# Performance work log

Hardware: AMD Instinct MI355X
Metric: run time of the kernel (lower is better)

Reference implementation:

```python
import jax, jax.numpy as jnp
import numpy as np

B, T, D = 32, 1024, 192
HIDDEN = 4
CH = D * HIDDEN          # conv hidden channels = in_channel * hidden_size
K1, K2 = 5, 3
PAD = 3                  # (K1 - 1) // 2 + 1 for odd kernel_size=5 (ReplicationPad1d)
NUM_LEVELS = 3
N_NODES = 2 ** NUM_LEVELS - 1  # 7 Interaction blocks in the SCINet tree
OUT_LEN = 512


def setup_inputs() -> dict:
    key = jax.random.key(0)
    ks = jax.random.split(key, 6)
    s1 = 1.0 / np.sqrt(D * K1)   # torch Conv1d default init bound (fan_in = Cin*k)
    s2 = 1.0 / np.sqrt(CH * K2)
    sp = 1.0 / np.sqrt(T)
    x = jax.random.normal(ks[0], (B, T, D), dtype=jnp.float32)
    # Stacked params for all 7 tree nodes x 4 branches (phi, psi, eta, rho)
    W1 = jax.random.uniform(ks[1], (N_NODES, 4, CH, D, K1), jnp.float32, -s1, s1)
    b1 = jax.random.uniform(ks[2], (N_NODES, 4, CH), jnp.float32, -s1, s1)
    W2 = jax.random.uniform(ks[3], (N_NODES, 4, D, CH, K2), jnp.float32, -s2, s2)
    b2 = jax.random.uniform(ks[4], (N_NODES, 4, D), jnp.float32, -s2, s2)
    # projection1 = Conv1d(input_len, output_len, k=1, bias=False) over time-as-channels
    Wproj = jax.random.uniform(ks[5], (OUT_LEN, T), jnp.float32, -sp, sp)
    return {"x": x, "W1": W1, "b1": b1, "W2": W2, "b2": b2, "Wproj": Wproj}


def _conv1d(x, w, b):
    # x: (B, Cin, L), w: (Cout, Cin, K)
    y = jax.lax.conv_general_dilated(x, w, (1,), 'VALID',
                                     dimension_numbers=('NCH', 'OIH', 'NCH'))
    return y + b[None, :, None]


def _branch(x, w1, b1, w2, b2):
    # ReplicationPad1d(3,3) -> Conv(k=5) -> LeakyReLU -> (Dropout p=0) -> Conv(k=3) -> Tanh
    xp = jnp.pad(x, ((0, 0), (0, 0), (PAD, PAD)), mode='edge')
    h = jax.nn.leaky_relu(_conv1d(xp, w1, b1), 0.01)
    return jnp.tanh(_conv1d(h, w2, b2))  # length back to L


def _interact(x, w1, b1, w2, b2):
    # x: (B, T, D) -> even/odd (B, D, T/2)
    xe = jnp.transpose(x[:, ::2, :], (0, 2, 1))
    xo = jnp.transpose(x[:, 1::2, :], (0, 2, 1))
    d = xo * jnp.exp(_branch(xe, w1[0], b1[0], w2[0], b2[0]))  # phi
    c = xe * jnp.exp(_branch(xo, w1[1], b1[1], w2[1], b2[1]))  # psi
    even_up = c + _branch(d, w1[2], b1[2], w2[2], b2[2])        # eta
    odd_up = d - _branch(c, w1[3], b1[3], w2[3], b2[3])         # rho
    return jnp.transpose(even_up, (0, 2, 1)), jnp.transpose(odd_up, (0, 2, 1))


def _zip_up(even, odd):
    # interleave even/odd along time (equal lengths since T % 2**levels == 0)
    b, t, c = even.shape
    return jnp.stack([even, odd], axis=2).reshape(b, 2 * t, c)


def _tree(x, level, idx, W1, b1, W2, b2):
    i = idx[0]
    idx[0] += 1
    e, o = _interact(x, W1[i], b1[i], W2[i], b2[i])
    if level == 0:
        return _zip_up(e, o)
    return _zip_up(_tree(e, level - 1, idx, W1, b1, W2, b2),
                   _tree(o, level - 1, idx, W1, b1, W2, b2))


def reference(x, W1, b1, W2, b2, Wproj):
    out = _tree(x, NUM_LEVELS - 1, [0], W1, b1, W2, b2) + x  # residual
    # projection1: Conv1d over time-as-channels, kernel 1, no bias
    return jnp.einsum('btd,ot->bod', out, Wproj)
```

## Files before the change

### kernel.cpp

```cpp
#include <hip/hip_runtime.h>
#include <hip/hip_bf16.h>

typedef unsigned short u16;
typedef unsigned int u32;
typedef __bf16 bf16x8 __attribute__((ext_vector_type(8)));
typedef float f32x4 __attribute__((ext_vector_type(4)));

#define NB 32
#define NT 1024
#define ND 192
#define NCH 768
#define NOUT 512

__device__ __forceinline__ float bf2f(u16 x) { return __uint_as_float(((u32)x) << 16); }
__device__ __forceinline__ u16 f2bf(float f) {
    u32 u = __float_as_uint(f);
    return (u16)((u + 0x7fffu + ((u >> 16) & 1u)) >> 16);
}
__device__ __forceinline__ float tanh_fast(float x) {
    float e = __expf(2.f * x);
    return 1.f - 2.f / (e + 1.f);
}

__constant__ int NODE_IDX[3][4] = {{0, 0, 0, 0}, {1, 4, 0, 0}, {2, 5, 3, 6}};

__global__ void cvt8(const float* __restrict__ in, u16* __restrict__ out, int n8) {
    int i = blockIdx.x * 256 + threadIdx.x;
    if (i >= n8) return;
    const float4* p = (const float4*)in + 2 * (size_t)i;
    float4 a = p[0], c = p[1];
    uint4 o;
    o.x = f2bf(a.x) | ((u32)f2bf(a.y) << 16);
    o.y = f2bf(a.z) | ((u32)f2bf(a.w) << 16);
    o.z = f2bf(c.x) | ((u32)f2bf(c.y) << 16);
    o.w = f2bf(c.z) | ((u32)f2bf(c.w) << 16);
    ((uint4*)out)[i] = o;
}

__global__ __launch_bounds__(256) void w1fk(const float* __restrict__ W1, u16* __restrict__ W1f) {
    __shared__ u16 ls[32][968];
    const int nb = blockIdx.x / 24;
    const int cot = blockIdx.x % 24;
    const float* src = W1 + ((size_t)nb * NCH + cot * 32) * (ND * 5);
    for (int idx = threadIdx.x; idx < 7680; idx += 256) {
        int e4 = idx * 4;
        int rowc = e4 / 960, col = e4 % 960;
        float4 v = *(const float4*)(src + (size_t)rowc * 960 + col);
        ls[rowc][col + 0] = f2bf(v.x);
        ls[rowc][col + 1] = f2bf(v.y);
        ls[rowc][col + 2] = f2bf(v.z);
        ls[rowc][col + 3] = f2bf(v.w);
    }
    __syncthreads();
    const int lane = threadIdx.x & 63, sub = threadIdx.x >> 6;
    const int g = lane >> 4, r = lane & 15;
    for (int it = 0; it < 15; ++it) {
        int fid = it * 4 + sub;
        int kkb = fid >> 1, cobl = fid & 1;
        u16 tmp[8];
#pragma unroll
        for (int e = 0; e < 8; ++e) {
            int kk = kkb * 32 + 8 * g + e;
            int ci = kk % 192, k = kk / 192;
            tmp[e] = ls[cobl * 16 + r][ci * 5 + k];
        }
        uint4 o;
        o.x = tmp[0] | ((u32)tmp[1] << 16);
        o.y = tmp[2] | ((u32)tmp[3] << 16);
        o.z = tmp[4] | ((u32)tmp[5] << 16);
        o.w = tmp[6] | ((u32)tmp[7] << 16);
        size_t off = (((size_t)nb * 30 + kkb) * 48 + cot * 2 + cobl) * 512 + lane * 8;
        *(uint4*)(W1f + off) = o;
    }
}

__global__ __launch_bounds__(256) void w2fk(const float* __restrict__ W2, u16* __restrict__ W2f) {
    __shared__ u16 ls[16][1160];
    const int ch = blockIdx.x & 1;
    const int t = blockIdx.x >> 1;
    const int nb = t / 12, cot = t % 12;
    const float* src = W2 + ((size_t)nb * ND + cot * 16) * (NCH * 3) + ch * 1152;
    for (int idx = threadIdx.x; idx < 4608; idx += 256) {
        int e4 = idx * 4;
        int rowc = e4 / 1152, col = e4 % 1152;
        float4 v = *(const float4*)(src + (size_t)rowc * (NCH * 3) + col);
        ls[rowc][col + 0] = f2bf(v.x);
        ls[rowc][col + 1] = f2bf(v.y);
        ls[rowc][col + 2] = f2bf(v.z);
        ls[rowc][col + 3] = f2bf(v.w);
    }
    __syncthreads();
    const int lane = threadIdx.x & 63, sub = threadIdx.x >> 6;
    const int g = lane >> 4, r = lane & 15;
    for (int it = 0; it < 9; ++it) {
        int fid = it * 4 + sub;
        int k = fid / 12, cib = fid % 12;
        int kkb = k * 24 + ch * 12 + cib;
        u16 tmp[8];
#pragma unroll
        for (int e = 0; e < 8; ++e) {
            int cl = cib * 32 + 8 * g + e;
            tmp[e] = ls[r][cl * 3 + k];
        }
        uint4 o;
        o.x = tmp[0] | ((u32)tmp[1] << 16);
        o.y = tmp[2] | ((u32)tmp[3] << 16);
        o.z = tmp[4] | ((u32)tmp[5] << 16);
        o.w = tmp[6] | ((u32)tmp[7] << 16);
        size_t off = (((size_t)nb * 72 + kkb) * 12 + cot) * 512 + lane * 8;
        *(uint4*)(W2f + off) = o;
    }
}

__global__ __launch_bounds__(256) void conv1m(
    const u16* __restrict__ bufb, const u16* __restrict__ dbufb, const u16* __restrict__ cbufb,
    const u16* __restrict__ W1f, const float* __restrict__ b1,
    u16* __restrict__ h, int lvl, int stage) {
    const int L = 512 >> lvl, nodes = 1 << lvl, Lout = L + 2;
    const int tid = threadIdx.x;
    const int cot = blockIdx.x % 6;
    const int mt = blockIdx.x / 6;
    const int z = blockIdx.z;
    const int g_node = z & (nodes - 1);
    const int br = z >> lvl;
    const int nb4 = NODE_IDX[lvl][g_node] * 4 + (stage ? 2 + br : br);

    const int r0 = mt * 128;
    const int b0 = r0 / Lout;
    const int t00 = r0 - b0 * Lout;
    const int s = Lout - t00;
    const int rowsValid0 = NB * Lout - r0;
    const int rowsValid = rowsValid0 < 128 ? rowsValid0 : 128;

    __shared__ u16 xs[136 * 192];

    const u16* dcb = br ? cbufb : dbufb;
    const int slot = g_node + (br << lvl);
    for (int ch = tid; ch < 136 * 24; ch += 256) {
        int j = ch / 24, c8 = ch % 24;
        int bb, u;
        if (j <= s + 3) { bb = b0; u = t00 - 3 + j; }
        else            { bb = b0 + 1; u = j - s - 7; }
        u = u < 0 ? 0 : (u > L - 1 ? L - 1 : u);
        if (bb > NB - 1) bb = NB - 1;
        const u16* p;
        if (stage == 0)
            p = bufb + ((size_t)bb * NT + slot + (size_t)u * (2 * nodes)) * ND + c8 * 8;
        else
            p = dcb + (((size_t)g_node * NB + bb) * L + u) * (size_t)ND + c8 * 8;
        *(uint4*)(xs + j * 192 + ((c8 * 8) ^ ((j & 7) << 3))) = *(const uint4*)p;
    }
    __syncthreads();

    const int lane = tid & 63, w = tid >> 6;
    const int wrow = w >> 1, wcol = w & 1;
    const int lr = lane & 15, lg = lane >> 4;

    int rowb[4];
#pragma unroll
    for (int m = 0; m < 4; ++m) {
        int i = wrow * 64 + m * 16 + lr;
        rowb[m] = i + (i >= s ? 4 : 0);
    }
    const u16* wf = W1f + (size_t)nb4 * 30 * 48 * 512 + (size_t)(cot * 8 + wcol * 4) * 512 + lane * 8;

    f32x4 acc[4][4];
    f32x4 zz = {0.f, 0.f, 0.f, 0.f};
#pragma unroll
    for (int m = 0; m < 4; ++m)
#pragma unroll
        for (int n = 0; n < 4; ++n) acc[m][n] = zz;

    auto loadA = [&](bf16x8(&dst)[4], int step) {
        const int k = step / 6, cib = step % 6;
#pragma unroll
        for (int m = 0; m < 4; ++m) {
            int row = rowb[m] + k;
            int idx = row * 192 + ((cib * 32 + lg * 8) ^ ((row & 7) << 3));
            dst[m] = *(const bf16x8*)(xs + idx);
        }
    };
    auto loadB = [&](bf16x8(&dst)[4], int step) {
#pragma unroll
        for (int n = 0; n < 4; ++n)
            dst[n] = *(const bf16x8*)(wf + ((size_t)step * 48 + n) * 512);
    };
    auto domfma = [&](bf16x8(&A)[4], bf16x8(&B)[4]) {
#pragma unroll
        for (int m = 0; m < 4; ++m)
#pragma unroll
            for (int n = 0; n < 4; ++n)
                acc[m][n] = __builtin_amdgcn_mfma_f32_16x16x32_bf16(A[m], B[n], acc[m][n], 0, 0, 0);
    };

    bf16x8 aE[4], bE[4], aO[4], bO[4];
    loadA(aE, 0); loadB(bE, 0);
#pragma unroll
    for (int sp = 0; sp < 15; ++sp) {
        loadA(aO, 2 * sp + 1); loadB(bO, 2 * sp + 1);
        domfma(aE, bE);
        if (sp < 14) { loadA(aE, 2 * sp + 2); loadB(bE, 2 * sp + 2); }
        domfma(aO, bO);
    }

    float bias[4];
    const float* bb1 = b1 + (size_t)nb4 * NCH + cot * 128 + wcol * 64 + lr;
#pragma unroll
    for (int n = 0; n < 4; ++n) bias[n] = bb1[n * 16];
    u16* hz = h + (size_t)z * NB * Lout * NCH;
#pragma unroll
    for (int m = 0; m < 4; ++m) {
#pragma unroll
        for (int rr = 0; rr < 4; ++rr) {
            int i = wrow * 64 + m * 16 + lg * 4 + rr;
            if (i < rowsValid) {
                int cross = (i >= s) ? 1 : 0;
                int bb = b0 + cross;
                int tt = cross ? i - s : t00 + i;
                u16* dst = hz + ((size_t)bb * Lout + tt) * NCH + cot * 128 + wcol * 64 + lr;
#pragma unroll
                for (int n = 0; n < 4; ++n) {
                    float v = acc[m][n][rr] + bias[n];
                    v = v > 0.f ? v : 0.01f * v;
                    dst[n * 16] = f2bf(v);
                }
            }
        }
    }
}

__global__ __launch_bounds__(256) void conv2m(
    u16* __restrict__ bufb, u16* __restrict__ dbufb, u16* __restrict__ cbufb,
    const u16* __restrict__ W2f, const float* __restrict__ b2,
    const u16* __restrict__ h, int lvl, int stage) {
    const int L = 512 >> lvl, nodes = 1 << lvl, Lout = L + 2;
    const int tid = threadIdx.x;
    const int mt = blockIdx.x;
    const int nh = blockIdx.y;
    const int z = blockIdx.z;
    const int g_node = z & (nodes - 1);
    const int br = z >> lvl;
    const int nb4 = NODE_IDX[lvl][g_node] * 4 + (stage ? 2 + br : br);
    const int r0 = mt * 64;
    const int b = r0 >> (9 - lvl);
    const int t0 = r0 & (L - 1);

    __shared__ u16 xs[66 * 192];
    const u16* hz = h + ((size_t)z * NB + b) * Lout * NCH;

    const int lane = tid & 63, w = tid >> 6;
    const int wrow = w >> 1, wcol = w & 1;
    const int lr = lane & 15, lg = lane >> 4;
    int rowb[2];
#pragma unroll
    for (int m = 0; m < 2; ++m) rowb[m] = wrow * 32 + m * 16 + lr;
    const u16* wf = W2f + (size_t)nb4 * 72 * 12 * 512 + (size_t)(nh * 6 + wcol * 3) * 512 + lane * 8;

    f32x4 acc[2][3];
    f32x4 zz = {0.f, 0.f, 0.f, 0.f};
#pragma unroll
    for (int m = 0; m < 2; ++m)
#pragma unroll
        for (int n = 0; n < 3; ++n) acc[m][n] = zz;

    for (int cc = 0; cc < 4; ++cc) {
        __syncthreads();
        for (int ch = tid; ch < 66 * 24; ch += 256) {
            int j = ch / 24, c8 = ch % 24;
            *(uint4*)(xs + j * 192 + ((c8 * 8) ^ ((j & 7) << 3))) =
                *(const uint4*)(hz + (size_t)(t0 + j) * NCH + cc * 192 + c8 * 8);
        }
        __syncthreads();

        auto loadA = [&](bf16x8(&dst)[2], int step) {
            const int k = step / 6, cib = step % 6;
#pragma unroll
            for (int m = 0; m < 2; ++m) {
                int row = rowb[m] + k;
                int idx = row * 192 + ((cib * 32 + lg * 8) ^ ((row & 7) << 3));
                dst[m] = *(const bf16x8*)(xs + idx);
            }
        };
        auto loadB = [&](bf16x8(&dst)[3], int step) {
            const int k = step / 6, cib = step % 6;
            const size_t kb = (size_t)(cc * 6 + k * 24 + cib) * 12 * 512;
#pragma unroll
            for (int n = 0; n < 3; ++n)
                dst[n] = *(const bf16x8*)(wf + kb + (size_t)n * 512);
        };
        auto domfma = [&](bf16x8(&A)[2], bf16x8(&B)[3]) {
#pragma unroll
            for (int m = 0; m < 2; ++m)
#pragma unroll
                for (int n = 0; n < 3; ++n)
                    acc[m][n] = __builtin_amdgcn_mfma_f32_16x16x32_bf16(A[m], B[n], acc[m][n], 0, 0, 0);
        };

        bf16x8 aE[2], bE[3], aO[2], bO[3];
        loadA(aE, 0); loadB(bE, 0);
#pragma unroll
        for (int sp = 0; sp < 9; ++sp) {
            loadA(aO, 2 * sp + 1); loadB(bO, 2 * sp + 1);
            domfma(aE, bE);
            if (sp < 8) { loadA(aE, 2 * sp + 2); loadB(bE, 2 * sp + 2); }
            domfma(aO, bO);
        }
    }

    float bias[3];
    const float* bb2 = b2 + (size_t)nb4 * ND + nh * 96 + wcol * 48 + lr;
#pragma unroll
    for (int n = 0; n < 3; ++n) bias[n] = bb2[n * 16];

    const int tstr = 2 * nodes;
    if (stage == 0) {
        const int mo = g_node + (br == 0 ? nodes : 0);
        const u16* mult = bufb + ((size_t)b * NT + mo) * ND;
        u16* dst = (br == 0 ? dbufb : cbufb) + ((size_t)g_node * NB + b) * (size_t)L * ND;
#pragma unroll
        for (int m = 0; m < 2; ++m) {
#pragma unroll
            for (int rr = 0; rr < 4; ++rr) {
                int i = wrow * 32 + m * 16 + lg * 4 + rr;
                int t = t0 + i;
#pragma unroll
                for (int n = 0; n < 3; ++n) {
                    int co = nh * 96 + wcol * 48 + n * 16 + lr;
                    float v = tanh_fast(acc[m][n][rr] + bias[n]);
                    float mlt = bf2f(mult[(size_t)t * tstr * ND + co]);
                    dst[(size_t)t * ND + co] = f2bf(mlt * __expf(v));
                }
            }
        }
    } else {
        const u16* other = (br == 0 ? cbufb : dbufb) + ((size_t)g_node * NB + b) * (size_t)L * ND;
        const int to = g_node + (br ? nodes : 0);
        u16* dst = bufb + ((size_t)b * NT + to) * ND;
#pragma unroll
        for (int m = 0; m < 2; ++m) {
#pragma unroll
            for (int rr = 0; rr < 4; ++rr) {
                int i = wrow * 32 + m * 16 + lg * 4 + rr;
                int t = t0 + i;
#pragma unroll
                for (int n = 0; n < 3; ++n) {
                    int co = nh * 96 + wcol * 48 + n * 16 + lr;
                    float v = tanh_fast(acc[m][n][rr] + bias[n]);
                    float o = bf2f(other[(size_t)t * ND + co]);
                    dst[(size_t)t * tstr * ND + co] = f2bf(br == 0 ? o + v : o - v);
                }
            }
        }
    }
}

__global__ __launch_bounds__(256) void mkin2T(const u16* __restrict__ bufb,
                                              const float* __restrict__ x,
                                              u16* __restrict__ in2T) {
    __shared__ u16 ls[64][72];
    const int b = blockIdx.z, t0 = blockIdx.y * 64, d0 = blockIdx.x * 64;
    const int tid = threadIdx.x;
#pragma unroll
    for (int it = 0; it < 2; ++it) {
        int idx = tid + it * 256;
        int c8 = idx >> 6, row = idx & 63;
        size_t base = ((size_t)b * NT + t0 + row) * ND + d0 + c8 * 8;
        uint4 vb = *(const uint4*)(bufb + base);
        float4 x1 = *(const float4*)(x + base);
        float4 x2 = *(const float4*)(x + base + 4);
        const u16* vs = (const u16*)&vb;
        ls[c8 * 8 + 0][row] = f2bf(bf2f(vs[0]) + x1.x);
        ls[c8 * 8 + 1][row] = f2bf(bf2f(vs[1]) + x1.y);
        ls[c8 * 8 + 2][row] = f2bf(bf2f(vs[2]) + x1.z);
        ls[c8 * 8 + 3][row] = f2bf(bf2f(vs[3]) + x1.w);
        ls[c8 * 8 + 4][row] = f2bf(bf2f(vs[4]) + x2.x);
        ls[c8 * 8 + 5][row] = f2bf(bf2f(vs[5]) + x2.y);
        ls[c8 * 8 + 6][row] = f2bf(bf2f(vs[6]) + x2.z);
        ls[c8 * 8 + 7][row] = f2bf(bf2f(vs[7]) + x2.w);
    }
    __syncthreads();
#pragma unroll
    for (int it = 0; it < 2; ++it) {
        int idx = tid + it * 256;
        int dl = idx >> 3, t8 = idx & 7;
        uint4 v = *(uint4*)&ls[dl][t8 * 8];
        *(uint4*)(in2T + ((size_t)b * ND + d0 + dl) * NT + t0 + t8 * 8) = v;
    }
}

__global__ __launch_bounds__(256) void projm(const u16* __restrict__ in2T,
                                             const u16* __restrict__ Wpb,
                                             float* __restrict__ out) {
    const int b = blockIdx.y, ot = blockIdx.x;
    const int tid = threadIdx.x, lane = tid & 63, w = tid >> 6;
    const int lr = lane & 15, lg = lane >> 4;
    const u16* ap = Wpb + ((size_t)(ot * 32 + lr)) * NT + lg * 8;
    const u16* bp = in2T + ((size_t)b * ND + w * 48 + lr) * NT + lg * 8;

    f32x4 acc[2][3];
    f32x4 zz = {0.f, 0.f, 0.f, 0.f};
#pragma unroll
    for (int m = 0; m < 2; ++m)
#pragma unroll
        for (int n = 0; n < 3; ++n) acc[m][n] = zz;

    auto loadA = [&](bf16x8(&dst)[2], int kkb) {
#pragma unroll
        for (int m = 0; m < 2; ++m)
            dst[m] = *(const bf16x8*)(ap + (size_t)m * 16 * NT + kkb * 32);
    };
    auto loadB = [&](bf16x8(&dst)[3], int kkb) {
#pragma unroll
        for (int n = 0; n < 3; ++n)
            dst[n] = *(const bf16x8*)(bp + (size_t)n * 16 * NT + kkb * 32);
    };
    auto domfma = [&](bf16x8(&A)[2], bf16x8(&B)[3]) {
#pragma unroll
        for (int m = 0; m < 2; ++m)
#pragma unroll
            for (int n = 0; n < 3; ++n)
                acc[m][n] = __builtin_amdgcn_mfma_f32_16x16x32_bf16(A[m], B[n], acc[m][n], 0, 0, 0);
    };

    bf16x8 aE[2], bE[3], aO[2], bO[3];
    loadA(aE, 0); loadB(bE, 0);
#pragma unroll
    for (int sp = 0; sp < 16; ++sp) {
        loadA(aO, 2 * sp + 1); loadB(bO, 2 * sp + 1);
        domfma(aE, bE);
        if (sp < 15) { loadA(aE, 2 * sp + 2); loadB(bE, 2 * sp + 2); }
        domfma(aO, bO);
    }

#pragma unroll
    for (int m = 0; m < 2; ++m)
#pragma unroll
        for (int rr = 0; rr < 4; ++rr) {
            int o = ot * 32 + m * 16 + lg * 4 + rr;
#pragma unroll
            for (int n = 0; n < 3; ++n) {
                int d = w * 48 + n * 16 + lr;
                out[((size_t)b * NOUT + o) * ND + d] = acc[m][n][rr];
            }
        }
}

extern "C" void kernel_launch(void* const* d_in, const int* in_sizes, int n_in,
                              void* d_out, int out_size, void* d_ws, size_t ws_size,
                              hipStream_t stream) {
    const float* x = (const float*)d_in[0];
    const float* W1 = (const float*)d_in[1];
    const float* b1 = (const float*)d_in[2];
    const float* W2 = (const float*)d_in[3];
    const float* b2 = (const float*)d_in[4];
    const float* Wp = (const float*)d_in[5];
    float* out = (float*)d_out;

    char* wsb = (char*)d_ws;
    size_t off = 0;
    auto carve = [&](size_t bytes) {
        void* p = wsb + off;
        off += (bytes + 255) & ~(size_t)255;
        return p;
    };
    const size_t w1f_e = (size_t)28 * 30 * 48 * 512;
    const size_t w2f_e = (size_t)28 * 72 * 12 * 512;
    const size_t wpb_e = (size_t)NOUT * NT;
    const size_t buf_e = (size_t)NB * NT * ND;
    const size_t dc_e = (size_t)NB * 512 * ND;
    const size_t h_e = (size_t)1040 * NB * NCH;
    const size_t i2_e = (size_t)NB * ND * NT;

    u16* W1f = (u16*)carve(sizeof(u16) * w1f_e);
    u16* W2f = (u16*)carve(sizeof(u16) * w2f_e);
    u16* Wpb = (u16*)carve(sizeof(u16) * wpb_e);
    u16* bufb = (u16*)carve(sizeof(u16) * buf_e);
    u16* dbufb = (u16*)carve(sizeof(u16) * dc_e);
    u16* cbufb = (u16*)carve(sizeof(u16) * dc_e);
    u16* h = (u16*)carve(sizeof(u16) * h_e);
    u16* in2T = (u16*)carve(sizeof(u16) * i2_e);
    if (off > ws_size) return;

    cvt8<<<(int)(buf_e / 8 / 256), 256, 0, stream>>>(x, bufb, (int)(buf_e / 8));
    cvt8<<<(int)(wpb_e / 8 / 256), 256, 0, stream>>>(Wp, Wpb, (int)(wpb_e / 8));
    w1fk<<<28 * 24, 256, 0, stream>>>(W1, W1f);
    w2fk<<<28 * 12 * 2, 256, 0, stream>>>(W2, W2f);

    for (int lvl = 0; lvl < 3; ++lvl) {
        int L = 512 >> lvl, nodes = 1 << lvl, Lout = L + 2;
        int mT1 = (NB * Lout + 127) / 128;
        dim3 g1(6 * mT1, 1, 2 * nodes);
        dim3 g2(NB * L / 64, 2, 2 * nodes);
        conv1m<<<g1, 256, 0, stream>>>(bufb, dbufb, cbufb, W1f, b1, h, lvl, 0);
        conv2m<<<g2, 256, 0, stream>>>(bufb, dbufb, cbufb, W2f, b2, h, lvl, 0);
        conv1m<<<g1, 256, 0, stream>>>(bufb, dbufb, cbufb, W1f, b1, h, lvl, 1);
        conv2m<<<g2, 256, 0, stream>>>(bufb, dbufb, cbufb, W2f, b2, h, lvl, 1);
    }
    mkin2T<<<dim3(3, 16, NB), 256, 0, stream>>>(bufb, x, in2T);
    projm<<<dim3(16, NB), 256, 0, stream>>>(in2T, Wpb, out);
}
```

Before: 799.4 us.

## Shrink conv1 M-tile, add XCD-aware block swizzle, and deepen B prefetch

conv1m's row tile drops from 128 to 64, so each of the four waves covers all 64 rows and 32 output channels. This halves LDS use and doubles the block count. Both conv kernels now use a flattened 1D grid with an XCD swizzle, so consecutive work-groups that share weights land on the same XCD L2. All three GEMM loops switch to a 3-deep B / 2-deep A register prefetch pipeline. The trade-offs are smaller MFMA tiles per wave in conv1, which means more A-tile reloads from LDS per FLOP, and higher register pressure from the deeper prefetch.

```diff
diff --git a/kernel.cpp b/kernel.cpp
--- a/kernel.cpp
+++ b/kernel.cpp
@@ -20,6 +20,11 @@
 __device__ __forceinline__ float tanh_fast(float x) {
     float e = __expf(2.f * x);
     return 1.f - 2.f / (e + 1.f);
+}
+__device__ __forceinline__ int xcd_swz(int bx, int nwg) {
+    int q = nwg >> 3, r = nwg & 7;
+    int xcd = bx & 7, idx = bx >> 3;
+    return (xcd < r ? xcd * (q + 1) : r * (q + 1) + (xcd - r) * q) + idx;
 }
 
 __constant__ int NODE_IDX[3][4] = {{0, 0, 0, 0}, {1, 4, 0, 0}, {2, 5, 3, 6}};
@@ -118,25 +123,28 @@
     u16* __restrict__ h, int lvl, int stage) {
     const int L = 512 >> lvl, nodes = 1 << lvl, Lout = L + 2;
     const int tid = threadIdx.x;
-    const int cot = blockIdx.x % 6;
-    const int mt = blockIdx.x / 6;
-    const int z = blockIdx.z;
+    const int mT1 = (NB * Lout + 63) / 64;
+    const int wg = xcd_swz(blockIdx.x, gridDim.x);
+    const int z = wg / (6 * mT1);
+    const int rem = wg - z * 6 * mT1;
+    const int mt = rem / 6;
+    const int cot = rem % 6;
     const int g_node = z & (nodes - 1);
     const int br = z >> lvl;
     const int nb4 = NODE_IDX[lvl][g_node] * 4 + (stage ? 2 + br : br);
 
-    const int r0 = mt * 128;
+    const int r0 = mt * 64;
     const int b0 = r0 / Lout;
     const int t00 = r0 - b0 * Lout;
     const int s = Lout - t00;
     const int rowsValid0 = NB * Lout - r0;
-    const int rowsValid = rowsValid0 < 128 ? rowsValid0 : 128;
-
-    __shared__ u16 xs[136 * 192];
+    const int rowsValid = rowsValid0 < 64 ? rowsValid0 : 64;
+
+    __shared__ u16 xs[72 * 192];
 
     const u16* dcb = br ? cbufb : dbufb;
     const int slot = g_node + (br << lvl);
-    for (int ch = tid; ch < 136 * 24; ch += 256) {
+    for (int ch = tid; ch < 72 * 24; ch += 256) {
         int j = ch / 24, c8 = ch % 24;
         int bb, u;
         if (j <= s + 3) { bb = b0; u = t00 - 3 + j; }
@@ -153,23 +161,22 @@
     __syncthreads();
 
     const int lane = tid & 63, w = tid >> 6;
-    const int wrow = w >> 1, wcol = w & 1;
     const int lr = lane & 15, lg = lane >> 4;
 
     int rowb[4];
 #pragma unroll
     for (int m = 0; m < 4; ++m) {
-        int i = wrow * 64 + m * 16 + lr;
+        int i = m * 16 + lr;
         rowb[m] = i + (i >= s ? 4 : 0);
     }
-    const u16* wf = W1f + (size_t)nb4 * 30 * 48 * 512 + (size_t)(cot * 8 + wcol * 4) * 512 + lane * 8;
-
-    f32x4 acc[4][4];
+    const u16* wf = W1f + (size_t)nb4 * 30 * 48 * 512 + (size_t)(cot * 8 + w * 2) * 512 + lane * 8;
+
+    f32x4 acc[4][2];
     f32x4 zz = {0.f, 0.f, 0.f, 0.f};
 #pragma unroll
     for (int m = 0; m < 4; ++m)
 #pragma unroll
-        for (int n = 0; n < 4; ++n) acc[m][n] = zz;
+        for (int n = 0; n < 2; ++n) acc[m][n] = zz;
 
     auto loadA = [&](bf16x8(&dst)[4], int step) {
         const int k = step / 6, cib = step % 6;
@@ -180,46 +187,47 @@
             dst[m] = *(const bf16x8*)(xs + idx);
         }
     };
-    auto loadB = [&](bf16x8(&dst)[4], int step) {
-#pragma unroll
-        for (int n = 0; n < 4; ++n)
+    auto loadB = [&](bf16x8(&dst)[2], int step) {
+#pragma unroll
+        for (int n = 0; n < 2; ++n)
             dst[n] = *(const bf16x8*)(wf + ((size_t)step * 48 + n) * 512);
     };
-    auto domfma = [&](bf16x8(&A)[4], bf16x8(&B)[4]) {
+    auto domfma = [&](bf16x8(&A)[4], bf16x8(&B)[2]) {
 #pragma unroll
         for (int m = 0; m < 4; ++m)
 #pragma unroll
-            for (int n = 0; n < 4; ++n)
+            for (int n = 0; n < 2; ++n)
                 acc[m][n] = __builtin_amdgcn_mfma_f32_16x16x32_bf16(A[m], B[n], acc[m][n], 0, 0, 0);
     };
 
-    bf16x8 aE[4], bE[4], aO[4], bO[4];
-    loadA(aE, 0); loadB(bE, 0);
-#pragma unroll
-    for (int sp = 0; sp < 15; ++sp) {
-        loadA(aO, 2 * sp + 1); loadB(bO, 2 * sp + 1);
-        domfma(aE, bE);
-        if (sp < 14) { loadA(aE, 2 * sp + 2); loadB(bE, 2 * sp + 2); }
-        domfma(aO, bO);
-    }
-
-    float bias[4];
-    const float* bb1 = b1 + (size_t)nb4 * NCH + cot * 128 + wcol * 64 + lr;
-#pragma unroll
-    for (int n = 0; n < 4; ++n) bias[n] = bb1[n * 16];
+    bf16x8 Ab[2][4], Bb[3][2];
+    loadA(Ab[0], 0);
+    loadB(Bb[0], 0);
+    loadB(Bb[1], 1);
+#pragma unroll
+    for (int sp = 0; sp < 30; ++sp) {
+        if (sp + 2 < 30) loadB(Bb[(sp + 2) % 3], sp + 2);
+        if (sp + 1 < 30) loadA(Ab[(sp + 1) & 1], sp + 1);
+        domfma(Ab[sp & 1], Bb[sp % 3]);
+    }
+
+    float bias[2];
+    const float* bb1 = b1 + (size_t)nb4 * NCH + cot * 128 + w * 32 + lr;
+#pragma unroll
+    for (int n = 0; n < 2; ++n) bias[n] = bb1[n * 16];
     u16* hz = h + (size_t)z * NB * Lout * NCH;
 #pragma unroll
     for (int m = 0; m < 4; ++m) {
 #pragma unroll
         for (int rr = 0; rr < 4; ++rr) {
-            int i = wrow * 64 + m * 16 + lg * 4 + rr;
+            int i = m * 16 + lg * 4 + rr;
             if (i < rowsValid) {
                 int cross = (i >= s) ? 1 : 0;
                 int bb = b0 + cross;
                 int tt = cross ? i - s : t00 + i;
-                u16* dst = hz + ((size_t)bb * Lout + tt) * NCH + cot * 128 + wcol * 64 + lr;
-#pragma unroll
-                for (int n = 0; n < 4; ++n) {
+                u16* dst = hz + ((size_t)bb * Lout + tt) * NCH + cot * 128 + w * 32 + lr;
+#pragma unroll
+                for (int n = 0; n < 2; ++n) {
                     float v = acc[m][n][rr] + bias[n];
                     v = v > 0.f ? v : 0.01f * v;
                     dst[n * 16] = f2bf(v);
@@ -235,9 +243,12 @@
     const u16* __restrict__ h, int lvl, int stage) {
     const int L = 512 >> lvl, nodes = 1 << lvl, Lout = L + 2;
     const int tid = threadIdx.x;
-    const int mt = blockIdx.x;
-    const int nh = blockIdx.y;
-    const int z = blockIdx.z;
+    const int nM = (NB * L) >> 6;
+    const int wg = xcd_swz(blockIdx.x, gridDim.x);
+    const int z = wg / (nM * 2);
+    const int rem = wg - z * nM * 2;
+    const int mt = rem >> 1;
+    const int nh = rem & 1;
     const int g_node = z & (nodes - 1);
     const int br = z >> lvl;
     const int nb4 = NODE_IDX[lvl][g_node] * 4 + (stage ? 2 + br : br);
@@ -296,14 +307,15 @@
                     acc[m][n] = __builtin_amdgcn_mfma_f32_16x16x32_bf16(A[m], B[n], acc[m][n], 0, 0, 0);
         };
 
-        bf16x8 aE[2], bE[3], aO[2], bO[3];
-        loadA(aE, 0); loadB(bE, 0);
-#pragma unroll
-        for (int sp = 0; sp < 9; ++sp) {
-            loadA(aO, 2 * sp + 1); loadB(bO, 2 * sp + 1);
-            domfma(aE, bE);
-            if (sp < 8) { loadA(aE, 2 * sp + 2); loadB(bE, 2 * sp + 2); }
-            domfma(aO, bO);
+        bf16x8 Ab[2][2], Bb[3][3];
+        loadA(Ab[0], 0);
+        loadB(Bb[0], 0);
+        loadB(Bb[1], 1);
+#pragma unroll
+        for (int sp = 0; sp < 18; ++sp) {
+            if (sp + 2 < 18) loadB(Bb[(sp + 2) % 3], sp + 2);
+            if (sp + 1 < 18) loadA(Ab[(sp + 1) & 1], sp + 1);
+            domfma(Ab[sp & 1], Bb[sp % 3]);
         }
     }
 
@@ -422,14 +434,15 @@
                 acc[m][n] = __builtin_amdgcn_mfma_f32_16x16x32_bf16(A[m], B[n], acc[m][n], 0, 0, 0);
     };
 
-    bf16x8 aE[2], bE[3], aO[2], bO[3];
-    loadA(aE, 0); loadB(bE, 0);
-#pragma unroll
-    for (int sp = 0; sp < 16; ++sp) {
-        loadA(aO, 2 * sp + 1); loadB(bO, 2 * sp + 1);
-        domfma(aE, bE);
-        if (sp < 15) { loadA(aE, 2 * sp + 2); loadB(bE, 2 * sp + 2); }
-        domfma(aO, bO);
+    bf16x8 Ab[2][2], Bb[3][3];
+    loadA(Ab[0], 0);
+    loadB(Bb[0], 0);
+    loadB(Bb[1], 1);
+#pragma unroll
+    for (int sp = 0; sp < 32; ++sp) {
+        if (sp + 2 < 32) loadB(Bb[(sp + 2) % 3], sp + 2);
+        if (sp + 1 < 32) loadA(Ab[(sp + 1) & 1], sp + 1);
+        domfma(Ab[sp & 1], Bb[sp % 3]);
     }
 
 #pragma unroll
@@ -488,9 +501,10 @@
 
     for (int lvl = 0; lvl < 3; ++lvl) {
         int L = 512 >> lvl, nodes = 1 << lvl, Lout = L + 2;
-        int mT1 = (NB * Lout + 127) / 128;
-        dim3 g1(6 * mT1, 1, 2 * nodes);
-        dim3 g2(NB * L / 64, 2, 2 * nodes);
+        int mT1 = (NB * Lout + 63) / 64;
+        int nM = NB * L / 64;
+        dim3 g1(6 * mT1 * 2 * nodes);
+        dim3 g2(nM * 2 * 2 * nodes);
         conv1m<<<g1, 256, 0, stream>>>(bufb, dbufb, cbufb, W1f, b1, h, lvl, 0);
         conv2m<<<g2, 256, 0, stream>>>(bufb, dbufb, cbufb, W2f, b2, h, lvl, 0);
         conv1m<<<g1, 256, 0, stream>>>(bufb, dbufb, cbufb, W1f, b1, h, lvl, 1);
```

New measurement: 778.4 us. -2.6%, faster.
